# Performance work log

Measured on AMD Instinct MI355X. Metric: run time of the kernel, lower is better.

Reference implementation:

```python
import jax, jax.numpy as jnp
import numpy as np

B, V, E, L, D = 16, 19, 361, 256, 64  # batch, vertices, edges/graph, seq_len, d_model
F_IN = 2 * D + 1  # concat(src_feat, tgt_feat, edge_weight)


def _linear_init(key, fan_in, fan_out):
    bound = 1.0 / np.sqrt(fan_in)
    kw, kb = jax.random.split(key)
    W = jax.random.uniform(kw, (fan_in, fan_out), jnp.float32, -bound, bound)
    b = jax.random.uniform(kb, (fan_out,), jnp.float32, -bound, bound)
    return W, b


def setup_inputs() -> dict:
    key = jax.random.key(0)
    ks = jax.random.split(key, 6)
    hidden_states = jax.random.normal(ks[0], (B * V, L, D), jnp.float32)
    edge_index = jax.random.randint(ks[1], (2, B * E, L), 0, B * V, dtype=jnp.int32)
    edge_weight = jax.random.uniform(ks[2], (B * E, L), jnp.float32)
    W1, b1 = _linear_init(ks[3], F_IN, D)
    W2, b2 = _linear_init(ks[4], D, D // 2)
    W3, b3 = _linear_init(ks[5], D // 2, 1)
    skip_param = jnp.float32(0.25)
    return {"hidden_states": hidden_states, "edge_weight": edge_weight,
            "W1": W1, "b1": b1, "W2": W2, "b2": b2, "W3": W3, "b3": b3,
            "skip_param": skip_param, "edge_index": edge_index}


def reference(hidden_states, edge_weight, W1, b1, W2, b2, W3, b3, skip_param, edge_index):
    # hidden_states: (B*V, L, D) -> (B, L, V, D) for per-timestep node gather
    hs = hidden_states.reshape(B, V, L, D).transpose(0, 2, 1, 3)
    # edge indices are global node ids; local vertex id = idx % V (as in torch code)
    src = (edge_index[0] % V).reshape(B, E, L).transpose(0, 2, 1)  # (B, L, E)
    tgt = (edge_index[1] % V).reshape(B, E, L).transpose(0, 2, 1)
    ew = edge_weight.reshape(B, E, L).transpose(0, 2, 1)           # (B, L, E)
    src_feat = jnp.take_along_axis(hs, src[..., None], axis=2)    # (B, L, E, D)
    tgt_feat = jnp.take_along_axis(hs, tgt[..., None], axis=2)    # (B, L, E, D)
    x = jnp.concatenate([src_feat, tgt_feat, ew[..., None]], axis=-1)  # (B, L, E, 2D+1)
    h = jax.nn.silu(x @ W1 + b1)
    h = jax.nn.silu(h @ W2 + b2)
    w = jax.nn.sigmoid((h @ W3 + b3)[..., 0])                     # (B, L, E)
    new_ew = skip_param * ew + (1.0 - skip_param) * w
    return new_ew.transpose(0, 2, 1).reshape(B * E, L)            # (B*E, L)
```

## Files before the change

### kernel.cpp

```cpp
#include <hip/hip_runtime.h>

#define NB 16
#define NV 19
#define NE 361
#define NL 256
#define ND 64
#define NTP 24
#define NEP (NTP * 16)
#define ASTRIDE 136

typedef __attribute__((ext_vector_type(8))) short bf16x8;
typedef __attribute__((ext_vector_type(4))) float f32x4;
typedef __attribute__((ext_vector_type(2))) __bf16 bf16v2;

union bf8u { unsigned u[4]; bf16x8 v; uint4 q; };

__device__ __forceinline__ unsigned pack_bf16(float lo, float hi) {
    bf16v2 v; v.x = (__bf16)lo; v.y = (__bf16)hi;
    return __builtin_bit_cast(unsigned, v);
}
__device__ __forceinline__ short f2bf(float f) {
    __bf16 h = (__bf16)f;
    return __builtin_bit_cast(short, h);
}
__device__ __forceinline__ float bflo(unsigned u) {
    return __builtin_bit_cast(float, u << 16);
}
__device__ __forceinline__ float bfhi(unsigned u) {
    return __builtin_bit_cast(float, u & 0xffff0000u);
}
__device__ __forceinline__ f32x4 silu4(f32x4 x) {
    f32x4 t = x * -1.44269504f;
    f32x4 d;
    d.x = __builtin_amdgcn_exp2f(t.x);
    d.y = __builtin_amdgcn_exp2f(t.y);
    d.z = __builtin_amdgcn_exp2f(t.z);
    d.w = __builtin_amdgcn_exp2f(t.w);
    d += 1.f;
    f32x4 r;
    r.x = __builtin_amdgcn_rcpf(d.x);
    r.y = __builtin_amdgcn_rcpf(d.y);
    r.z = __builtin_amdgcn_rcpf(d.z);
    r.w = __builtin_amdgcn_rcpf(d.w);
    return x * r;
}
__device__ __forceinline__ float sigm(float x) {
    return __builtin_amdgcn_rcpf(1.f + __builtin_amdgcn_exp2f(x * -1.44269504f));
}

__global__ __launch_bounds__(256, 5) void edge_learner_kernel(
    const float* __restrict__ hs,
    const float* __restrict__ ew_in,
    const float* __restrict__ W1,
    const float* __restrict__ b1,
    const float* __restrict__ W2,
    const float* __restrict__ b2,
    const float* __restrict__ W3,
    const float* __restrict__ b3,
    const float* __restrict__ skip_p,
    const int*   __restrict__ eidx,
    float* __restrict__ out)
{
    __shared__ __align__(16) short A_s[NV * ASTRIDE];
    __shared__ __align__(8)  uint2 meta_s[NEP];

    const int tid  = threadIdx.x;
    const int lane = tid & 63;
    const int wave = tid >> 6;
    const int lq   = lane >> 4;
    const int lm   = lane & 15;
    const int bid0 = blockIdx.x;
    const int bid  = (bid0 & 7) * 512 + (bid0 >> 3);
    const int b    = bid >> 8;
    const int l    = bid & 255;

    for (int e = tid; e < NEP; e += 256) {
        uint2 m;
        if (e < NE) {
            size_t row = (size_t)(b * NE + e) * NL + l;
            unsigned so = (unsigned)((eidx[row] % NV) * ASTRIDE);
            unsigned to = (unsigned)((eidx[(size_t)NB * NE * NL + row] % NV) * ASTRIDE + 64);
            m.x = so | (to << 16);
            m.y = __builtin_bit_cast(unsigned, ew_in[row]);
        } else {
            m.x = 64u << 16; m.y = 0u;
        }
        meta_s[e] = m;
    }

    f32x4 w1lv[2][2];
    #pragma unroll
    for (int ks = 0; ks < 2; ++ks) {
        w1lv[ks][0] = *(const f32x4*)&W1[128 * 64 + ks * 32 + lq * 8];
        w1lv[ks][1] = *(const f32x4*)&W1[128 * 64 + ks * 32 + lq * 8 + 4];
    }
    bf8u w2f[2][2];
    #pragma unroll
    for (int nt = 0; nt < 2; ++nt)
        #pragma unroll
        for (int ks = 0; ks < 2; ++ks) {
            const float* w2p = &W2[(ks * 32 + lq * 8) * 32 + nt * 16 + lm];
            #pragma unroll
            for (int p = 0; p < 4; ++p)
                w2f[nt][ks].u[p] = pack_bf16(w2p[(2 * p) * 32], w2p[(2 * p + 1) * 32]);
        }
    const f32x4 b2v0 = *(const f32x4*)&b2[lq * 4];
    const f32x4 b2v1 = *(const f32x4*)&b2[16 + lq * 4];
    const f32x4 w3v0 = *(const f32x4*)&W3[lq * 4];
    const f32x4 w3v1 = *(const f32x4*)&W3[16 + lq * 4];
    const float b3v  = b3[0];
    const float skip = skip_p[0];

    {
        const int half = wave >> 1;
        const int oc0  = (wave & 1) * 32;
        const float hb0 = 0.5f * b1[(wave * 32 + lm) & 63];
        const float hb1 = 0.5f * b1[(wave * 32 + 16 + lm) & 63];
        bf8u w1f[2][2];
        #pragma unroll
        for (int nt = 0; nt < 2; ++nt)
            #pragma unroll
            for (int ks = 0; ks < 2; ++ks) {
                const float* wp = &W1[(half * 64 + ks * 32 + lq * 8) * 64
                                      + oc0 + nt * 16 + lm];
                #pragma unroll
                for (int p = 0; p < 4; ++p)
                    w1f[nt][ks].u[p] = pack_bf16(wp[(2 * p) * 64], wp[(2 * p + 1) * 64]);
            }

        f32x4 acc00 = {0,0,0,0}, acc01 = {0,0,0,0}, acc10 = {0,0,0,0}, acc11 = {0,0,0,0};
        #pragma unroll
        for (int Mt = 0; Mt < 2; ++Mt) {
            int v  = Mt * 16 + lm;
            int vc = v < NV ? v : NV - 1;
            const float* hp = hs + ((size_t)(b * NV + vc) * NL + l) * ND;
            bf8u af[2];
            #pragma unroll
            for (int ks = 0; ks < 2; ++ks) {
                float4 x0 = *(const float4*)&hp[ks * 32 + lq * 8];
                float4 x1 = *(const float4*)&hp[ks * 32 + lq * 8 + 4];
                af[ks].u[0] = pack_bf16(x0.x, x0.y);
                af[ks].u[1] = pack_bf16(x0.z, x0.w);
                af[ks].u[2] = pack_bf16(x1.x, x1.y);
                af[ks].u[3] = pack_bf16(x1.z, x1.w);
            }
            if (Mt == 0) {
                acc00 = __builtin_amdgcn_mfma_f32_16x16x32_bf16(af[0].v, w1f[0][0].v, acc00, 0, 0, 0);
                acc00 = __builtin_amdgcn_mfma_f32_16x16x32_bf16(af[1].v, w1f[0][1].v, acc00, 0, 0, 0);
                acc01 = __builtin_amdgcn_mfma_f32_16x16x32_bf16(af[0].v, w1f[1][0].v, acc01, 0, 0, 0);
                acc01 = __builtin_amdgcn_mfma_f32_16x16x32_bf16(af[1].v, w1f[1][1].v, acc01, 0, 0, 0);
            } else {
                acc10 = __builtin_amdgcn_mfma_f32_16x16x32_bf16(af[0].v, w1f[0][0].v, acc10, 0, 0, 0);
                acc10 = __builtin_amdgcn_mfma_f32_16x16x32_bf16(af[1].v, w1f[0][1].v, acc10, 0, 0, 0);
                acc11 = __builtin_amdgcn_mfma_f32_16x16x32_bf16(af[0].v, w1f[1][0].v, acc11, 0, 0, 0);
                acc11 = __builtin_amdgcn_mfma_f32_16x16x32_bf16(af[1].v, w1f[1][1].v, acc11, 0, 0, 0);
            }
        }
        #pragma unroll
        for (int r = 0; r < 4; ++r) {
            int v0 = lq * 4 + r;
            A_s[v0 * ASTRIDE + wave * 32 + lm]      = f2bf(acc00[r] + hb0);
            A_s[v0 * ASTRIDE + wave * 32 + 16 + lm] = f2bf(acc01[r] + hb1);
            int v1 = 16 + lq * 4 + r;
            if (v1 < NV) {
                A_s[v1 * ASTRIDE + wave * 32 + lm]      = f2bf(acc10[r] + hb0);
                A_s[v1 * ASTRIDE + wave * 32 + 16 + lm] = f2bf(acc11[r] + hb1);
            }
        }
    }
    __syncthreads();

    #pragma unroll
    for (int i = 0; i < 6; ++i) {
        const int t = wave + 4 * i;
        const uint2 m = meta_s[t * 16 + lm];
        const int so = (int)(m.x & 0xffffu);
        const int to = (int)(m.x >> 16);
        const float ew = __builtin_bit_cast(float, m.y);

        bf8u a1[2];
        #pragma unroll
        for (int ks = 0; ks < 2; ++ks) {
            const uint4 as = *(const uint4*)&A_s[so + ks * 32 + lq * 8];
            const uint4 at = *(const uint4*)&A_s[to + ks * 32 + lq * 8];
            f32x4 x0, x1;
            x0.x = bflo(as.x) + bflo(at.x);
            x0.y = bfhi(as.x) + bfhi(at.x);
            x0.z = bflo(as.y) + bflo(at.y);
            x0.w = bfhi(as.y) + bfhi(at.y);
            x1.x = bflo(as.z) + bflo(at.z);
            x1.y = bfhi(as.z) + bfhi(at.z);
            x1.z = bflo(as.w) + bflo(at.w);
            x1.w = bfhi(as.w) + bfhi(at.w);
            x0 += ew * w1lv[ks][0];
            x1 += ew * w1lv[ks][1];
            f32x4 y0 = silu4(x0);
            f32x4 y1 = silu4(x1);
            a1[ks].u[0] = pack_bf16(y0.x, y0.y);
            a1[ks].u[1] = pack_bf16(y0.z, y0.w);
            a1[ks].u[2] = pack_bf16(y1.x, y1.y);
            a1[ks].u[3] = pack_bf16(y1.z, y1.w);
        }

        f32x4 c0 = {0,0,0,0}, c1 = {0,0,0,0};
        c0 = __builtin_amdgcn_mfma_f32_16x16x32_bf16(w2f[0][0].v, a1[0].v, c0, 0, 0, 0);
        c0 = __builtin_amdgcn_mfma_f32_16x16x32_bf16(w2f[0][1].v, a1[1].v, c0, 0, 0, 0);
        c1 = __builtin_amdgcn_mfma_f32_16x16x32_bf16(w2f[1][0].v, a1[0].v, c1, 0, 0, 0);
        c1 = __builtin_amdgcn_mfma_f32_16x16x32_bf16(w2f[1][1].v, a1[1].v, c1, 0, 0, 0);

        f32x4 h0 = silu4(c0 + b2v0);
        f32x4 h1 = silu4(c1 + b2v1);
        f32x4 pv = h0 * w3v0 + h1 * w3v1;
        float p  = (pv.x + pv.y) + (pv.z + pv.w);
        p += __shfl_xor(p, 16);
        p += __shfl_xor(p, 32);

        if (lane < 16) {
            int er = t * 16 + lane;
            if (er < NE) {
                float wgt = sigm(p + b3v);
                out[(size_t)(b * NE + er) * NL + l] = skip * ew + (1.f - skip) * wgt;
            }
        }
    }
}

extern "C" void kernel_launch(void* const* d_in, const int* in_sizes, int n_in,
                              void* d_out, int out_size, void* d_ws, size_t ws_size,
                              hipStream_t stream) {
    const float* hs   = (const float*)d_in[0];
    const float* ew   = (const float*)d_in[1];
    const float* W1   = (const float*)d_in[2];
    const float* b1   = (const float*)d_in[3];
    const float* W2   = (const float*)d_in[4];
    const float* b2   = (const float*)d_in[5];
    const float* W3   = (const float*)d_in[6];
    const float* b3   = (const float*)d_in[7];
    const float* skip = (const float*)d_in[8];
    const int*   eidx = (const int*)d_in[9];
    float* outp = (float*)d_out;

    dim3 grid(NB * NL);
    dim3 block(256);
    hipLaunchKernelGGL(edge_learner_kernel, grid, block, 0, stream,
                       hs, ew, W1, b1, W2, b2, W3, b3, skip, eidx, outp);
}
```

Measured before the change: 57.27 us.

## Split per-node W1 projection into separate kernel writing bf16 workspace

Moves the per-vertex first-layer projection (hs @ W1 halves plus bias) out of the edge kernel into a new build_A_kernel. That kernel processes 16 timesteps per block so the MFMA M-dimension is fully used, where the old per-timestep tiles padded 19 vertices up to 32. It writes bf16 results to global workspace, which the edge kernel then copies into shared memory. The edge kernel becomes lighter and its occupancy hint rises. The cost is a second launch and an extra global round trip of about 10 MB of bf16.

```diff
diff --git a/kernel.cpp b/kernel.cpp
--- a/kernel.cpp
+++ b/kernel.cpp
@@ -8,6 +8,7 @@
 #define NTP 24
 #define NEP (NTP * 16)
 #define ASTRIDE 136
+#define ACOLS 128
 
 typedef __attribute__((ext_vector_type(8))) short bf16x8;
 typedef __attribute__((ext_vector_type(4))) float f32x4;
@@ -48,11 +49,74 @@
     return __builtin_amdgcn_rcpf(1.f + __builtin_amdgcn_exp2f(x * -1.44269504f));
 }
 
-__global__ __launch_bounds__(256, 5) void edge_learner_kernel(
+__global__ __launch_bounds__(256, 4) void build_A_kernel(
     const float* __restrict__ hs,
+    const float* __restrict__ W1,
+    const float* __restrict__ b1,
+    short* __restrict__ A_out)
+{
+    const int tid  = threadIdx.x;
+    const int lane = tid & 63;
+    const int wave = tid >> 6;
+    const int lq   = lane >> 4;
+    const int lm   = lane & 15;
+    const int bid  = blockIdx.x;
+    const int vh   = bid & 3;
+    const int lc   = (bid >> 2) & 15;
+    const int b    = bid >> 6;
+    const int l0   = lc * 16;
+    const int v0   = vh * 5;
+    const int v1   = (vh == 3) ? NV : v0 + 5;
+
+    const int cg   = wave;
+    const int half = cg >> 1;
+    const int oc0  = (cg & 1) * 32;
+    const float hb0 = 0.5f * b1[(cg * 32 + lm) & 63];
+    const float hb1 = 0.5f * b1[(cg * 32 + 16 + lm) & 63];
+
+    bf8u w1f[2][2];
+    #pragma unroll
+    for (int nt = 0; nt < 2; ++nt)
+        #pragma unroll
+        for (int ks = 0; ks < 2; ++ks) {
+            const float* wp = &W1[(half * 64 + ks * 32 + lq * 8) * 64
+                                  + oc0 + nt * 16 + lm];
+            #pragma unroll
+            for (int p = 0; p < 4; ++p)
+                w1f[nt][ks].u[p] = pack_bf16(wp[(2 * p) * 64], wp[(2 * p + 1) * 64]);
+        }
+
+    for (int v = v0; v < v1; ++v) {
+        const float* hp = hs + ((size_t)(b * NV + v) * NL + l0 + lm) * ND;
+        bf8u af[2];
+        #pragma unroll
+        for (int ks = 0; ks < 2; ++ks) {
+            float4 x0 = *(const float4*)&hp[ks * 32 + lq * 8];
+            float4 x1 = *(const float4*)&hp[ks * 32 + lq * 8 + 4];
+            af[ks].u[0] = pack_bf16(x0.x, x0.y);
+            af[ks].u[1] = pack_bf16(x0.z, x0.w);
+            af[ks].u[2] = pack_bf16(x1.x, x1.y);
+            af[ks].u[3] = pack_bf16(x1.z, x1.w);
+        }
+        f32x4 a0 = {0,0,0,0}, a1 = {0,0,0,0};
+        a0 = __builtin_amdgcn_mfma_f32_16x16x32_bf16(af[0].v, w1f[0][0].v, a0, 0, 0, 0);
+        a0 = __builtin_amdgcn_mfma_f32_16x16x32_bf16(af[1].v, w1f[0][1].v, a0, 0, 0, 0);
+        a1 = __builtin_amdgcn_mfma_f32_16x16x32_bf16(af[0].v, w1f[1][0].v, a1, 0, 0, 0);
+        a1 = __builtin_amdgcn_mfma_f32_16x16x32_bf16(af[1].v, w1f[1][1].v, a1, 0, 0, 0);
+        #pragma unroll
+        for (int r = 0; r < 4; ++r) {
+            int dl = lq * 4 + r;
+            short* base = A_out + ((size_t)(b * NL + l0 + dl) * NV + v) * ACOLS + cg * 32;
+            base[lm]      = f2bf(a0[r] + hb0);
+            base[16 + lm] = f2bf(a1[r] + hb1);
+        }
+    }
+}
+
+__global__ __launch_bounds__(256, 6) void edge_learner_kernel(
+    const short* __restrict__ A_glob,
     const float* __restrict__ ew_in,
     const float* __restrict__ W1,
-    const float* __restrict__ b1,
     const float* __restrict__ W2,
     const float* __restrict__ b2,
     const float* __restrict__ W3,
@@ -88,6 +152,15 @@
         meta_s[e] = m;
     }
 
+    {
+        const uint4* Ag = (const uint4*)(A_glob + (size_t)bid * (NV * ACOLS));
+        for (int i = tid; i < NV * ACOLS / 8; i += 256) {
+            int v = i >> 4;
+            int c = (i & 15) * 8;
+            *(uint4*)&A_s[v * ASTRIDE + c] = Ag[i];
+        }
+    }
+
     f32x4 w1lv[2][2];
     #pragma unroll
     for (int ks = 0; ks < 2; ++ks) {
@@ -111,63 +184,6 @@
     const float b3v  = b3[0];
     const float skip = skip_p[0];
 
-    {
-        const int half = wave >> 1;
-        const int oc0  = (wave & 1) * 32;
-        const float hb0 = 0.5f * b1[(wave * 32 + lm) & 63];
-        const float hb1 = 0.5f * b1[(wave * 32 + 16 + lm) & 63];
-        bf8u w1f[2][2];
-        #pragma unroll
-        for (int nt = 0; nt < 2; ++nt)
-            #pragma unroll
-            for (int ks = 0; ks < 2; ++ks) {
-                const float* wp = &W1[(half * 64 + ks * 32 + lq * 8) * 64
-                                      + oc0 + nt * 16 + lm];
-                #pragma unroll
-                for (int p = 0; p < 4; ++p)
-                    w1f[nt][ks].u[p] = pack_bf16(wp[(2 * p) * 64], wp[(2 * p + 1) * 64]);
-            }
-
-        f32x4 acc00 = {0,0,0,0}, acc01 = {0,0,0,0}, acc10 = {0,0,0,0}, acc11 = {0,0,0,0};
-        #pragma unroll
-        for (int Mt = 0; Mt < 2; ++Mt) {
-            int v  = Mt * 16 + lm;
-            int vc = v < NV ? v : NV - 1;
-            const float* hp = hs + ((size_t)(b * NV + vc) * NL + l) * ND;
-            bf8u af[2];
-            #pragma unroll
-            for (int ks = 0; ks < 2; ++ks) {
-                float4 x0 = *(const float4*)&hp[ks * 32 + lq * 8];
-                float4 x1 = *(const float4*)&hp[ks * 32 + lq * 8 + 4];
-                af[ks].u[0] = pack_bf16(x0.x, x0.y);
-                af[ks].u[1] = pack_bf16(x0.z, x0.w);
-                af[ks].u[2] = pack_bf16(x1.x, x1.y);
-                af[ks].u[3] = pack_bf16(x1.z, x1.w);
-            }
-            if (Mt == 0) {
-                acc00 = __builtin_amdgcn_mfma_f32_16x16x32_bf16(af[0].v, w1f[0][0].v, acc00, 0, 0, 0);
-                acc00 = __builtin_amdgcn_mfma_f32_16x16x32_bf16(af[1].v, w1f[0][1].v, acc00, 0, 0, 0);
-                acc01 = __builtin_amdgcn_mfma_f32_16x16x32_bf16(af[0].v, w1f[1][0].v, acc01, 0, 0, 0);
-                acc01 = __builtin_amdgcn_mfma_f32_16x16x32_bf16(af[1].v, w1f[1][1].v, acc01, 0, 0, 0);
-            } else {
-                acc10 = __builtin_amdgcn_mfma_f32_16x16x32_bf16(af[0].v, w1f[0][0].v, acc10, 0, 0, 0);
-                acc10 = __builtin_amdgcn_mfma_f32_16x16x32_bf16(af[1].v, w1f[0][1].v, acc10, 0, 0, 0);
-                acc11 = __builtin_amdgcn_mfma_f32_16x16x32_bf16(af[0].v, w1f[1][0].v, acc11, 0, 0, 0);
-                acc11 = __builtin_amdgcn_mfma_f32_16x16x32_bf16(af[1].v, w1f[1][1].v, acc11, 0, 0, 0);
-            }
-        }
-        #pragma unroll
-        for (int r = 0; r < 4; ++r) {
-            int v0 = lq * 4 + r;
-            A_s[v0 * ASTRIDE + wave * 32 + lm]      = f2bf(acc00[r] + hb0);
-            A_s[v0 * ASTRIDE + wave * 32 + 16 + lm] = f2bf(acc01[r] + hb1);
-            int v1 = 16 + lq * 4 + r;
-            if (v1 < NV) {
-                A_s[v1 * ASTRIDE + wave * 32 + lm]      = f2bf(acc10[r] + hb0);
-                A_s[v1 * ASTRIDE + wave * 32 + 16 + lm] = f2bf(acc11[r] + hb1);
-            }
-        }
-    }
     __syncthreads();
 
     #pragma unroll
@@ -239,9 +255,10 @@
     const float* skip = (const float*)d_in[8];
     const int*   eidx = (const int*)d_in[9];
     float* outp = (float*)d_out;
-
-    dim3 grid(NB * NL);
-    dim3 block(256);
-    hipLaunchKernelGGL(edge_learner_kernel, grid, block, 0, stream,
-                       hs, ew, W1, b1, W2, b2, W3, b3, skip, eidx, outp);
-}
+    short* A_ws = (short*)d_ws;
+
+    hipLaunchKernelGGL(build_A_kernel, dim3(NB * 16 * 4), dim3(256), 0, stream,
+                       hs, W1, b1, A_ws);
+    hipLaunchKernelGGL(edge_learner_kernel, dim3(NB * NL), dim3(256), 0, stream,
+                       A_ws, ew, W1, W2, b2, W3, b3, skip, eidx, outp);
+}
```

New measurement: 69.89 us. 22.0% more time.

## Replace per-edge LDS gather with one-hot selection MFMA over transposed node projections

Applied to the files above, without the earlier changes.

The per-node layer-1 projections are stored transposed in LDS and loaded once into register fragments. Each edge's src+tgt gather and edge-weight term now come from MFMAs with one-hot bf16 selector vectors, with the edge-weight column of W1 placed in an unused slot. This removes per-edge LDS reads and scalar unpack/add work but adds eight MFMAs per tile, more registers, and lowers the occupancy hint from 5 to 4. The edge weight and the W1 edge column are now rounded to bf16 inside the MFMA, which changes precision slightly.

```diff
diff --git a/kernel.cpp b/kernel.cpp
--- a/kernel.cpp
+++ b/kernel.cpp
@@ -7,7 +7,7 @@
 #define ND 64
 #define NTP 24
 #define NEP (NTP * 16)
-#define ASTRIDE 136
+#define ATS 72
 
 typedef __attribute__((ext_vector_type(8))) short bf16x8;
 typedef __attribute__((ext_vector_type(4))) float f32x4;
@@ -22,12 +22,6 @@
 __device__ __forceinline__ short f2bf(float f) {
     __bf16 h = (__bf16)f;
     return __builtin_bit_cast(short, h);
-}
-__device__ __forceinline__ float bflo(unsigned u) {
-    return __builtin_bit_cast(float, u << 16);
-}
-__device__ __forceinline__ float bfhi(unsigned u) {
-    return __builtin_bit_cast(float, u & 0xffff0000u);
 }
 __device__ __forceinline__ f32x4 silu4(f32x4 x) {
     f32x4 t = x * -1.44269504f;
@@ -48,7 +42,7 @@
     return __builtin_amdgcn_rcpf(1.f + __builtin_amdgcn_exp2f(x * -1.44269504f));
 }
 
-__global__ __launch_bounds__(256, 5) void edge_learner_kernel(
+__global__ __launch_bounds__(256, 4) void edge_learner_kernel(
     const float* __restrict__ hs,
     const float* __restrict__ ew_in,
     const float* __restrict__ W1,
@@ -61,7 +55,7 @@
     const int*   __restrict__ eidx,
     float* __restrict__ out)
 {
-    __shared__ __align__(16) short A_s[NV * ASTRIDE];
+    __shared__ __align__(16) short A_T[64 * ATS];
     __shared__ __align__(8)  uint2 meta_s[NEP];
 
     const int tid  = threadIdx.x;
@@ -74,26 +68,25 @@
     const int b    = bid >> 8;
     const int l    = bid & 255;
 
+    for (int i = tid; i < 64 * ATS / 8; i += 256) {
+        uint4 z; z.x = 0; z.y = 0; z.z = 0; z.w = 0;
+        *(uint4*)&A_T[i * 8] = z;
+    }
+
     for (int e = tid; e < NEP; e += 256) {
         uint2 m;
         if (e < NE) {
             size_t row = (size_t)(b * NE + e) * NL + l;
-            unsigned so = (unsigned)((eidx[row] % NV) * ASTRIDE);
-            unsigned to = (unsigned)((eidx[(size_t)NB * NE * NL + row] % NV) * ASTRIDE + 64);
-            m.x = so | (to << 16);
+            unsigned s = (unsigned)(eidx[row] % NV);
+            unsigned t = (unsigned)(eidx[(size_t)NB * NE * NL + row] % NV);
+            m.x = s | (t << 16);
             m.y = __builtin_bit_cast(unsigned, ew_in[row]);
         } else {
-            m.x = 64u << 16; m.y = 0u;
+            m.x = 0; m.y = 0;
         }
         meta_s[e] = m;
     }
 
-    f32x4 w1lv[2][2];
-    #pragma unroll
-    for (int ks = 0; ks < 2; ++ks) {
-        w1lv[ks][0] = *(const f32x4*)&W1[128 * 64 + ks * 32 + lq * 8];
-        w1lv[ks][1] = *(const f32x4*)&W1[128 * 64 + ks * 32 + lq * 8 + 4];
-    }
     bf8u w2f[2][2];
     #pragma unroll
     for (int nt = 0; nt < 2; ++nt)
@@ -110,6 +103,10 @@
     const f32x4 w3v1 = *(const f32x4*)&W3[16 + lq * 4];
     const float b3v  = b3[0];
     const float skip = skip_p[0];
+
+    __syncthreads();
+
+    if (tid < 64) A_T[tid * ATS + 31] = f2bf(W1[128 * 64 + tid]);
 
     {
         const int half = wave >> 1;
@@ -156,51 +153,81 @@
                 acc11 = __builtin_amdgcn_mfma_f32_16x16x32_bf16(af[1].v, w1f[1][1].v, acc11, 0, 0, 0);
             }
         }
+        const int tr0 = (wave & 1) * 32 + lm;
+        const int tr1 = (wave & 1) * 32 + 16 + lm;
+        const int cof = (wave >> 1) * 32;
         #pragma unroll
         for (int r = 0; r < 4; ++r) {
             int v0 = lq * 4 + r;
-            A_s[v0 * ASTRIDE + wave * 32 + lm]      = f2bf(acc00[r] + hb0);
-            A_s[v0 * ASTRIDE + wave * 32 + 16 + lm] = f2bf(acc01[r] + hb1);
+            A_T[tr0 * ATS + cof + v0] = f2bf(acc00[r] + hb0);
+            A_T[tr1 * ATS + cof + v0] = f2bf(acc01[r] + hb1);
             int v1 = 16 + lq * 4 + r;
             if (v1 < NV) {
-                A_s[v1 * ASTRIDE + wave * 32 + lm]      = f2bf(acc10[r] + hb0);
-                A_s[v1 * ASTRIDE + wave * 32 + 16 + lm] = f2bf(acc11[r] + hb1);
+                A_T[tr0 * ATS + cof + v1] = f2bf(acc10[r] + hb0);
+                A_T[tr1 * ATS + cof + v1] = f2bf(acc11[r] + hb1);
             }
         }
     }
     __syncthreads();
+
+    bf8u afr[4][2];
+    #pragma unroll
+    for (int mt = 0; mt < 4; ++mt) {
+        const int c = (mt >> 1) * 32 + (mt & 1) * 4 + ((lm >> 2) << 3) + (lm & 3);
+        #pragma unroll
+        for (int kc = 0; kc < 2; ++kc)
+            afr[mt][kc].q = *(const uint4*)&A_T[c * ATS + kc * 32 + lq * 8];
+    }
 
     #pragma unroll
     for (int i = 0; i < 6; ++i) {
         const int t = wave + 4 * i;
         const uint2 m = meta_s[t * 16 + lm];
-        const int so = (int)(m.x & 0xffffu);
-        const int to = (int)(m.x >> 16);
+        const int src = (int)(m.x & 0xffffu);
+        const int tgt = (int)(m.x >> 16);
         const float ew = __builtin_bit_cast(float, m.y);
 
+        bf8u s0, s1;
+        {
+            const int base = lq * 8;
+            int w  = src - base;
+            int ix = w >> 1;
+            unsigned pat = (w & 1) ? 0x3F800000u : 0x3F80u;
+            s0.u[0] = (ix == 0) ? pat : 0u;
+            s0.u[1] = (ix == 1) ? pat : 0u;
+            s0.u[2] = (ix == 2) ? pat : 0u;
+            s0.u[3] = (ix == 3) ? pat : 0u;
+            unsigned ewm = (lq == 3) ? (((unsigned)(unsigned short)f2bf(ew)) << 16) : 0u;
+            s0.u[3] |= ewm;
+            int w2_ = tgt - base;
+            int ix2 = w2_ >> 1;
+            unsigned pat2 = (w2_ & 1) ? 0x3F800000u : 0x3F80u;
+            s1.u[0] = (ix2 == 0) ? pat2 : 0u;
+            s1.u[1] = (ix2 == 1) ? pat2 : 0u;
+            s1.u[2] = (ix2 == 2) ? pat2 : 0u;
+            s1.u[3] = (ix2 == 3) ? pat2 : 0u;
+        }
+
+        f32x4 z0 = {0,0,0,0}, z1 = {0,0,0,0}, z2 = {0,0,0,0}, z3 = {0,0,0,0};
+        z0 = __builtin_amdgcn_mfma_f32_16x16x32_bf16(afr[0][0].v, s0.v, z0, 0, 0, 0);
+        z0 = __builtin_amdgcn_mfma_f32_16x16x32_bf16(afr[0][1].v, s1.v, z0, 0, 0, 0);
+        z1 = __builtin_amdgcn_mfma_f32_16x16x32_bf16(afr[1][0].v, s0.v, z1, 0, 0, 0);
+        z1 = __builtin_amdgcn_mfma_f32_16x16x32_bf16(afr[1][1].v, s1.v, z1, 0, 0, 0);
+        z2 = __builtin_amdgcn_mfma_f32_16x16x32_bf16(afr[2][0].v, s0.v, z2, 0, 0, 0);
+        z2 = __builtin_amdgcn_mfma_f32_16x16x32_bf16(afr[2][1].v, s1.v, z2, 0, 0, 0);
+        z3 = __builtin_amdgcn_mfma_f32_16x16x32_bf16(afr[3][0].v, s0.v, z3, 0, 0, 0);
+        z3 = __builtin_amdgcn_mfma_f32_16x16x32_bf16(afr[3][1].v, s1.v, z3, 0, 0, 0);
+
+        f32x4 y0 = silu4(z0), y1 = silu4(z1), y2 = silu4(z2), y3 = silu4(z3);
         bf8u a1[2];
-        #pragma unroll
-        for (int ks = 0; ks < 2; ++ks) {
-            const uint4 as = *(const uint4*)&A_s[so + ks * 32 + lq * 8];
-            const uint4 at = *(const uint4*)&A_s[to + ks * 32 + lq * 8];
-            f32x4 x0, x1;
-            x0.x = bflo(as.x) + bflo(at.x);
-            x0.y = bfhi(as.x) + bfhi(at.x);
-            x0.z = bflo(as.y) + bflo(at.y);
-            x0.w = bfhi(as.y) + bfhi(at.y);
-            x1.x = bflo(as.z) + bflo(at.z);
-            x1.y = bfhi(as.z) + bfhi(at.z);
-            x1.z = bflo(as.w) + bflo(at.w);
-            x1.w = bfhi(as.w) + bfhi(at.w);
-            x0 += ew * w1lv[ks][0];
-            x1 += ew * w1lv[ks][1];
-            f32x4 y0 = silu4(x0);
-            f32x4 y1 = silu4(x1);
-            a1[ks].u[0] = pack_bf16(y0.x, y0.y);
-            a1[ks].u[1] = pack_bf16(y0.z, y0.w);
-            a1[ks].u[2] = pack_bf16(y1.x, y1.y);
-            a1[ks].u[3] = pack_bf16(y1.z, y1.w);
-        }
+        a1[0].u[0] = pack_bf16(y0.x, y0.y);
+        a1[0].u[1] = pack_bf16(y0.z, y0.w);
+        a1[0].u[2] = pack_bf16(y1.x, y1.y);
+        a1[0].u[3] = pack_bf16(y1.z, y1.w);
+        a1[1].u[0] = pack_bf16(y2.x, y2.y);
+        a1[1].u[1] = pack_bf16(y2.z, y2.w);
+        a1[1].u[2] = pack_bf16(y3.x, y3.y);
+        a1[1].u[3] = pack_bf16(y3.z, y3.w);
 
         f32x4 c0 = {0,0,0,0}, c1 = {0,0,0,0};
         c0 = __builtin_amdgcn_mfma_f32_16x16x32_bf16(w2f[0][0].v, a1[0].v, c0, 0, 0, 0);
```

Measured after the change: 57.81 us. Within noise of the previous version (+0.9%).
